# Performance work log

Measured on AMD Instinct MI355X. Metric: run time of the kernel, lower is better.

The kernel has to match this reference:

```python
import jax, jax.numpy as jnp
import numpy as np


def gcn_conv(x, edge_index, edge_weight, W, b):
    """PyG GCNConv: add self-loops (weight 1), symmetric normalization,
    linear transform, edge-weighted scatter-add aggregation, bias."""
    N = x.shape[0]
    src = jnp.concatenate([edge_index[0], jnp.arange(N, dtype=edge_index.dtype)])
    dst = jnp.concatenate([edge_index[1], jnp.arange(N, dtype=edge_index.dtype)])
    ew = jnp.concatenate([edge_weight, jnp.ones((N,), dtype=edge_weight.dtype)])
    # deg over destination nodes (source_to_target flow)
    deg = jax.ops.segment_sum(ew, dst, num_segments=N)
    dinv = jnp.where(deg > 0, deg ** -0.5, 0.0).astype(x.dtype)
    norm = dinv[src] * ew * dinv[dst]          # [E+N]
    xw = x @ W                                  # [N, out] linear first (cheaper)
    msgs = norm[:, None] * xw[src]              # [E+N, out]
    out = jax.ops.segment_sum(msgs, dst, num_segments=N)
    return out + b


def setup_inputs() -> dict:
    key = jax.random.key(0)
    ks = jax.random.split(key, 7)
    N, E, F_in, H, F_out = 100000, 1600000, 394, 256, 64
    x = jax.random.normal(ks[0], (N, F_in), dtype=jnp.float32)
    edge_index = jax.random.randint(ks[1], (2, E), 0, N, dtype=jnp.int32)
    edge_weight = jax.random.uniform(ks[2], (E,), dtype=jnp.float32)
    W1 = jax.random.normal(ks[3], (F_in, H), dtype=jnp.float32) * (1.0 / np.sqrt(F_in))
    b1 = jnp.zeros((H,), dtype=jnp.float32)
    W2 = jax.random.normal(ks[4], (H, F_out), dtype=jnp.float32) * (1.0 / np.sqrt(H))
    b2 = jnp.zeros((F_out,), dtype=jnp.float32)
    return {"x": x, "edge_index": edge_index, "edge_weight": edge_weight,
            "W1": W1, "b1": b1, "W2": W2, "b2": b2}


def reference(x, edge_index, edge_weight, W1, b1, W2, b2):
    h = gcn_conv(x, edge_index, edge_weight, W1, b1)
    h = jax.nn.relu(h)
    # F.dropout(training=self.training) is identity in eval mode
    out = gcn_conv(h, edge_index, edge_weight, W2, b2)
    return out
```

## Files before the change

### kernel.cpp

```cpp
#include <hip/hip_runtime.h>
#include <hip/hip_bf16.h>
#include <hip/hip_fp16.h>
#include <type_traits>


typedef _Float16 f16x8 __attribute__((ext_vector_type(8)));
typedef float f32x4 __attribute__((ext_vector_type(4)));

#define DEG_MASK ((1ull << 42) - 1)

__device__ inline void async_copy16(const void* g, void* l) {
    __builtin_amdgcn_global_load_lds(
        (const __attribute__((address_space(1))) void*)g,
        (__attribute__((address_space(3))) void*)l, 16, 0, 0);
}


__global__ __launch_bounds__(256) void init_node(unsigned long long* packed, int N) {
    int i = blockIdx.x * 256 + threadIdx.x;
    if (i < N) packed[i] = 0ull;
}

__global__ __launch_bounds__(256) void accum_deg_hist(const int* __restrict__ dst,
                                                      const float* __restrict__ ew,
                                                      unsigned long long* packed, int E) {
    int e = blockIdx.x * 256 + threadIdx.x;
    if (e < E) {
        int d = dst[e];
        unsigned long long add =
            (1ull << 42) + (unsigned long long)(ew[e] * 4294967296.0f);
        atomicAdd(&packed[d], add);
    }
}

#define SCAN_TILE 2048

__global__ __launch_bounds__(256) void scan1(const unsigned long long* __restrict__ packed,
                                             int* __restrict__ rowptr,
                                             float* __restrict__ dinv,
                                             int* __restrict__ bsums, int N) {
    __shared__ int tmp[256];
    int t = threadIdx.x;
    int base = blockIdx.x * SCAN_TILE + t * 8;
    int v[8], s = 0;
#pragma unroll
    for (int j = 0; j < 8; ++j) {
        int idx = base + j;
        if (idx < N) {
            unsigned long long pv = packed[idx];
            v[j] = (int)(pv >> 42);
            dinv[idx] = rsqrtf(1.0f + (float)(pv & DEG_MASK) * (1.0f / 4294967296.0f));
        } else v[j] = 0;
        s += v[j];
    }
    tmp[t] = s;
    __syncthreads();
#pragma unroll
    for (int off = 1; off < 256; off <<= 1) {
        int u = (t >= off) ? tmp[t - off] : 0;
        __syncthreads();
        tmp[t] += u;
        __syncthreads();
    }
    int run = tmp[t] - s;
#pragma unroll
    for (int j = 0; j < 8; ++j) {
        if (base + j < N) rowptr[base + j] = run;
        run += v[j];
    }
    if (t == 255) bsums[blockIdx.x] = tmp[255];
}

__global__ __launch_bounds__(256) void scan2(int* bsums, int* rowptr, int NB, int N, int E) {
    __shared__ int tmp[256];
    int t = threadIdx.x;
    int v = (t < NB) ? bsums[t] : 0;
    tmp[t] = v;
    __syncthreads();
#pragma unroll
    for (int off = 1; off < 256; off <<= 1) {
        int u = (t >= off) ? tmp[t - off] : 0;
        __syncthreads();
        tmp[t] += u;
        __syncthreads();
    }
    if (t < NB) bsums[t] = tmp[t] - v;
    if (t == 0) rowptr[N] = E;
}

__global__ __launch_bounds__(256) void scan3(int* rowptr, int* cursor,
                                             const int* __restrict__ bsums, int N) {
    int base = blockIdx.x * SCAN_TILE + threadIdx.x * 8;
    int off = bsums[blockIdx.x];
#pragma unroll
    for (int j = 0; j < 8; ++j)
        if (base + j < N) {
            int v = rowptr[base + j] + off;
            rowptr[base + j] = v;
            cursor[base + j] = v;
        }
}

__global__ __launch_bounds__(256) void fill_csr(const int* __restrict__ src,
                                                const int* __restrict__ dst,
                                                const float* __restrict__ ew,
                                                const float* __restrict__ dinv,
                                                int* __restrict__ cursor,
                                                int2* __restrict__ cv, int E) {
    int e = blockIdx.x * 256 + threadIdx.x;
    if (e < E) {
        int d = dst[e], s = src[e];
        int pos = atomicAdd(&cursor[d], 1);
        float v = dinv[s] * ew[e] * dinv[d];
        cv[pos] = make_int2(s, __float_as_int(v));
    }
}

__global__ __launch_bounds__(256) void tohalf_w(const float* __restrict__ W,
                                                __half* __restrict__ WT,
                                                int K, int N, int Kpad) {
    int idx = blockIdx.x * 256 + threadIdx.x;
    int total = N * Kpad;
    if (idx >= total) return;
    int n = idx / Kpad, k = idx % Kpad;
    float v = (k < K) ? W[(size_t)k * N + n] : 0.0f;
    WT[idx] = __float2half(v);
}

__global__ __launch_bounds__(256) void tohalf_x(const float* __restrict__ x,
                                                __half* __restrict__ Xh,
                                                int Nn, int K, int Kpad) {
    int idx = blockIdx.x * 256 + threadIdx.x;
    int cpr = Kpad / 8;
    int total = Nn * cpr;
    if (idx >= total) return;
    int row = idx / cpr, c = idx % cpr;
    int gk = c * 8;
    const float* p = x + (size_t)row * K + gk;
    float v[8];
    if (gk + 8 <= K) {
#pragma unroll
        for (int j = 0; j < 4; ++j) {
            float2 t2 = *(const float2*)(p + j * 2);
            v[j * 2] = t2.x; v[j * 2 + 1] = t2.y;
        }
    } else {
#pragma unroll
        for (int j = 0; j < 8; ++j) v[j] = (gk + j < K) ? p[j] : 0.0f;
    }
    union { __half2 h[4]; uint4 u; } pk;
#pragma unroll
    for (int j = 0; j < 4; ++j) pk.h[j] = __floats2half2_rn(v[j * 2], v[j * 2 + 1]);
    *(uint4*)&Xh[(size_t)row * Kpad + gk] = pk.u;
}

template <int BM, int BN, int WARPS_M, int WARPS_N, int NT>
__global__ __launch_bounds__(NT) void gemm_f16(const __half* __restrict__ Ah,
                                               const __half* __restrict__ BT,
                                               __half* __restrict__ C,
                                               int M, int Kpad) {
    const int WM = BM / WARPS_M, WN = BN / WARPS_N;
    const int FM = WM / 16, FN = WN / 16;
    const int ACH = BM * 4;
    const int BCH = BN * 4;
    const int TOTCH = ACH + BCH;
    const int CH = TOTCH / NT;
    static_assert(CH == 3, "vmcnt(3) hardcoded below");
    __shared__ __align__(16) __half lds[2][TOTCH * 8];

    int tid = threadIdx.x;
    int lane = tid & 63;
    int w = tid >> 6;
    int wr = w / WARPS_N, wc = w % WARPS_N;
    int bm = blockIdx.x * BM;
    int lrow = lane & 15;
    int lslot = lane >> 4;

    const __half* srcp[CH];
#pragma unroll
    for (int i = 0; i < CH; ++i) {
        int ch = tid + i * NT;
        if (ch < ACH) {
            int c = ch, row = c >> 2;
            int grow = bm + row;
            if (grow >= M) grow = M - 1;
            srcp[i] = Ah + (size_t)grow * Kpad + (size_t)(((c & 3) ^ ((row >> 1) & 3)) * 8);
        } else {
            int c = ch - ACH, row = c >> 2;
            srcp[i] = BT + (size_t)row * Kpad + (size_t)(((c & 3) ^ ((row >> 1) & 3)) * 8);
        }
    }

    f32x4 acc[FM][FN];
#pragma unroll
    for (int m = 0; m < FM; ++m)
#pragma unroll
        for (int n = 0; n < FN; ++n) acc[m][n] = (f32x4){0.f, 0.f, 0.f, 0.f};

    auto stage = [&](int buf) {
#pragma unroll
        for (int i = 0; i < CH; ++i) {
            async_copy16(srcp[i], &lds[buf][(size_t)((tid & ~63) + i * NT) * 8]);
            srcp[i] += 32;
        }
    };

    auto compute = [&](int buf) {
        f16x8 af[FM], bf[FN];
#pragma unroll
        for (int m = 0; m < FM; ++m) {
            int row = wr * WM + m * 16 + lrow;
            int p = lslot ^ ((row >> 1) & 3);
            af[m] = *(const f16x8*)&lds[buf][(size_t)(row * 4 + p) * 8];
        }
#pragma unroll
        for (int n = 0; n < FN; ++n) {
            int row = wc * WN + n * 16 + lrow;
            int p = lslot ^ ((row >> 1) & 3);
            bf[n] = *(const f16x8*)&lds[buf][(size_t)(ACH + row * 4 + p) * 8];
        }
#pragma unroll
        for (int m = 0; m < FM; ++m)
#pragma unroll
            for (int n = 0; n < FN; ++n)
                acc[m][n] = __builtin_amdgcn_mfma_f32_16x16x32_f16(af[m], bf[n], acc[m][n], 0, 0, 0);
    };

    const int nsteps = Kpad / 32;
    stage(0);
    for (int s = 0; s < nsteps; ++s) {
        if (s + 1 < nsteps) {
            stage((s + 1) & 1);
            asm volatile("s_waitcnt vmcnt(3)" ::: "memory");
        } else {
            asm volatile("s_waitcnt vmcnt(0)" ::: "memory");
        }
        __builtin_amdgcn_s_barrier();
        compute(s & 1);
        __builtin_amdgcn_s_barrier();
    }

    __syncthreads();
    {
        const int LW = WN + 8;
        __half* tile = (__half*)lds + (size_t)w * 16 * LW;
        const int CPR = WN / 8;
        const int CHT = (16 * CPR) / 64;
#pragma unroll
        for (int m = 0; m < FM; ++m) {
            int rb = bm + wr * WM + m * 16;
#pragma unroll
            for (int n = 0; n < FN; ++n)
#pragma unroll
                for (int i = 0; i < 4; ++i)
                    tile[((lane >> 4) * 4 + i) * LW + n * 16 + (lane & 15)] =
                        __float2half(acc[m][n][i]);
#pragma unroll
            for (int c = 0; c < CHT; ++c) {
                int ch = lane + c * 64;
                int r = ch / CPR, cc = ch % CPR;
                uint4 v = *(uint4*)&tile[r * LW + cc * 8];
                int grow = rb + r;
                if (grow < M)
                    *(uint4*)&C[(size_t)grow * BN + wc * WN + cc * 8] = v;
            }
        }
    }
}

template <int F, int LPN, int RELU, typename OutT>
__global__ __launch_bounds__(256) void gatherh(const int* __restrict__ rowptr,
                                               const int2* __restrict__ cv,
                                               const __half* __restrict__ xw,
                                               const float* __restrict__ dinv,
                                               const float* __restrict__ bias,
                                               OutT* __restrict__ out, int N) {
    const int NPB = 256 / LPN;
    int d = blockIdx.x * NPB + threadIdx.x / LPN;
    if (d >= N) return;
    int lane = threadIdx.x % LPN;

    float di = dinv[d];
    float w = di * di;
    uint2 raw = *(const uint2*)(xw + (size_t)d * F + lane * 4);
    float2 u0 = __half22float2(*(__half2*)&raw.x);
    float2 u1 = __half22float2(*(__half2*)&raw.y);
    float a0 = w * u0.x, a1 = w * u0.y, a2 = w * u1.x, a3 = w * u1.y;
    float b0 = 0.f, b1 = 0.f, b2 = 0.f, b3 = 0.f;

    int p = rowptr[d], p1 = rowptr[d + 1];
    for (; p + 4 <= p1; p += 4) {
        int2 e0 = cv[p], e1 = cv[p + 1], e2 = cv[p + 2], e3 = cv[p + 3];
        uint2 r0 = *(const uint2*)(xw + (size_t)e0.x * F + lane * 4);
        uint2 r1 = *(const uint2*)(xw + (size_t)e1.x * F + lane * 4);
        uint2 r2 = *(const uint2*)(xw + (size_t)e2.x * F + lane * 4);
        uint2 r3 = *(const uint2*)(xw + (size_t)e3.x * F + lane * 4);
        float w0 = __int_as_float(e0.y), w1 = __int_as_float(e1.y);
        float w2 = __int_as_float(e2.y), w3 = __int_as_float(e3.y);
        {
            float2 v0 = __half22float2(*(__half2*)&r0.x);
            float2 v1 = __half22float2(*(__half2*)&r0.y);
            a0 = fmaf(w0, v0.x, a0); a1 = fmaf(w0, v0.y, a1);
            a2 = fmaf(w0, v1.x, a2); a3 = fmaf(w0, v1.y, a3);
        }
        {
            float2 v0 = __half22float2(*(__half2*)&r1.x);
            float2 v1 = __half22float2(*(__half2*)&r1.y);
            b0 = fmaf(w1, v0.x, b0); b1 = fmaf(w1, v0.y, b1);
            b2 = fmaf(w1, v1.x, b2); b3 = fmaf(w1, v1.y, b3);
        }
        {
            float2 v0 = __half22float2(*(__half2*)&r2.x);
            float2 v1 = __half22float2(*(__half2*)&r2.y);
            a0 = fmaf(w2, v0.x, a0); a1 = fmaf(w2, v0.y, a1);
            a2 = fmaf(w2, v1.x, a2); a3 = fmaf(w2, v1.y, a3);
        }
        {
            float2 v0 = __half22float2(*(__half2*)&r3.x);
            float2 v1 = __half22float2(*(__half2*)&r3.y);
            b0 = fmaf(w3, v0.x, b0); b1 = fmaf(w3, v0.y, b1);
            b2 = fmaf(w3, v1.x, b2); b3 = fmaf(w3, v1.y, b3);
        }
    }
    for (; p < p1; ++p) {
        int2 e = cv[p];
        float wv = __int_as_float(e.y);
        uint2 rv = *(const uint2*)(xw + (size_t)e.x * F + lane * 4);
        float2 v0 = __half22float2(*(__half2*)&rv.x);
        float2 v1 = __half22float2(*(__half2*)&rv.y);
        a0 = fmaf(wv, v0.x, a0); a1 = fmaf(wv, v0.y, a1);
        a2 = fmaf(wv, v1.x, a2); a3 = fmaf(wv, v1.y, a3);
    }
    a0 += b0; a1 += b1; a2 += b2; a3 += b3;

    float4 bb = *(const float4*)&bias[lane * 4];
    a0 += bb.x; a1 += bb.y; a2 += bb.z; a3 += bb.w;
    if (RELU) {
        a0 = fmaxf(a0, 0.f); a1 = fmaxf(a1, 0.f);
        a2 = fmaxf(a2, 0.f); a3 = fmaxf(a3, 0.f);
    }
    if constexpr (std::is_same_v<OutT, float>) {
        *(float4*)&out[(size_t)d * F + lane * 4] = make_float4(a0, a1, a2, a3);
    } else {
        __half2 h0 = __floats2half2_rn(a0, a1);
        __half2 h1 = __floats2half2_rn(a2, a3);
        uint2 packed;
        packed.x = *(uint*)&h0;
        packed.y = *(uint*)&h1;
        *(uint2*)&out[(size_t)d * F + lane * 4] = packed;
    }
}

extern "C" void kernel_launch(void* const* d_in, const int* in_sizes, int n_in,
                              void* d_out, int out_size, void* d_ws, size_t ws_size,
                              hipStream_t stream) {
    const float* x  = (const float*)d_in[0];
    const int*   ei = (const int*)d_in[1];
    const float* ew = (const float*)d_in[2];
    const float* W1 = (const float*)d_in[3];
    const float* b1 = (const float*)d_in[4];
    const float* W2 = (const float*)d_in[5];
    const float* b2 = (const float*)d_in[6];
    float* out = (float*)d_out;

    const int H    = in_sizes[4];
    const int Fout = in_sizes[6];
    const int Fin  = in_sizes[3] / H;
    const int N    = in_sizes[0] / Fin;
    const int E    = in_sizes[2];

    const int Kpad1 = (Fin + 31) / 32 * 32;
    const int Kpad2 = (H + 31) / 32 * 32;

    const int* src = ei;
    const int* dst = ei + E;

    unsigned long long* packed = (unsigned long long*)d_ws;
    float* dinv   = (float*)(packed + N);
    int*   rowptr = (int*)(dinv + N);
    int*   cursor = rowptr + N + 4;
    int*   bsums  = cursor + N + 4;
    int2*  cv     = (int2*)(bsums + 256);
    __half* bufA  = (__half*)(cv + E);
    __half* bufB  = bufA + (size_t)N * H;
    __half* xh    = bufB + (size_t)N * H;
    __half* wt1   = xh + (size_t)N * Kpad1;
    __half* wt2   = wt1 + (size_t)H * Kpad1;

    const int NB = (N + SCAN_TILE - 1) / SCAN_TILE;

    init_node<<<(N + 255) / 256, 256, 0, stream>>>(packed, N);
    accum_deg_hist<<<(E + 255) / 256, 256, 0, stream>>>(dst, ew, packed, E);

    scan1<<<NB, 256, 0, stream>>>(packed, rowptr, dinv, bsums, N);
    scan2<<<1, 256, 0, stream>>>(bsums, rowptr, NB, N, E);
    scan3<<<NB, 256, 0, stream>>>(rowptr, cursor, bsums, N);
    fill_csr<<<(E + 255) / 256, 256, 0, stream>>>(src, dst, ew, dinv, cursor, cv, E);

    tohalf_w<<<(H * Kpad1 + 255) / 256, 256, 0, stream>>>(W1, wt1, Fin, H, Kpad1);
    tohalf_w<<<(Fout * Kpad2 + 255) / 256, 256, 0, stream>>>(W2, wt2, H, Fout, Kpad2);
    tohalf_x<<<((size_t)N * (Kpad1 / 8) + 255) / 256, 256, 0, stream>>>(x, xh, N, Fin, Kpad1);

    gemm_f16<128, 256, 2, 4, 512><<<(N + 127) / 128, 512, 0, stream>>>(xh, wt1, bufA, N, Kpad1);

    gatherh<256, 64, 1, __half><<<(N + 3) / 4, 256, 0, stream>>>(
        rowptr, cv, bufA, dinv, b1, bufB, N);

    gemm_f16<128, 64, 2, 2, 256><<<(N + 127) / 128, 256, 0, stream>>>(bufB, wt2, bufA, N, Kpad2);

    gatherh<64, 16, 0, float><<<(N + 15) / 16, 256, 0, stream>>>(
        rowptr, cv, bufA, dinv, b2, out, N);
}
```

Before: 476.3 us.

## Fuse fp32-to-fp16 conversion of x into first GEMM's A-tile loading

Removes the separate tohalf_x pass and its fp16 staging buffer. The first-layer GEMM now reads fp32 x rows directly into registers, converts them to fp16 and writes them into swizzled LDS, while B tiles still use async global-to-LDS copies. This saves a full write and re-read of the converted x matrix. In exchange, A loads go through registers with explicit waitcnt handling instead of the async LDS path, which could weaken latency hiding in the GEMM main loop.

Measured after the change: 466.8 us. 2.0% less time.

```diff
diff --git a/kernel.cpp b/kernel.cpp
--- a/kernel.cpp
+++ b/kernel.cpp
@@ -127,31 +127,145 @@
     WT[idx] = __float2half(v);
 }
 
-__global__ __launch_bounds__(256) void tohalf_x(const float* __restrict__ x,
-                                                __half* __restrict__ Xh,
-                                                int Nn, int K, int Kpad) {
-    int idx = blockIdx.x * 256 + threadIdx.x;
-    int cpr = Kpad / 8;
-    int total = Nn * cpr;
-    if (idx >= total) return;
-    int row = idx / cpr, c = idx % cpr;
-    int gk = c * 8;
-    const float* p = x + (size_t)row * K + gk;
-    float v[8];
-    if (gk + 8 <= K) {
-#pragma unroll
-        for (int j = 0; j < 4; ++j) {
-            float2 t2 = *(const float2*)(p + j * 2);
-            v[j * 2] = t2.x; v[j * 2 + 1] = t2.y;
-        }
-    } else {
-#pragma unroll
-        for (int j = 0; j < 8; ++j) v[j] = (gk + j < K) ? p[j] : 0.0f;
-    }
-    union { __half2 h[4]; uint4 u; } pk;
-#pragma unroll
-    for (int j = 0; j < 4; ++j) pk.h[j] = __floats2half2_rn(v[j * 2], v[j * 2 + 1]);
-    *(uint4*)&Xh[(size_t)row * Kpad + gk] = pk.u;
+template <int BM, int BN, int WARPS_M, int WARPS_N, int NT>
+__global__ __launch_bounds__(NT) void gemm_f32a(const float* __restrict__ Ax,
+                                                const __half* __restrict__ BT,
+                                                __half* __restrict__ C,
+                                                int M, int K, int Kpad) {
+    const int WM = BM / WARPS_M, WN = BN / WARPS_N;
+    const int FM = WM / 16, FN = WN / 16;
+    const int ACH = BM * 4;
+    const int BCH = BN * 4;
+    static_assert(ACH == NT, "1 A-chunk per thread");
+    static_assert(BCH == 2 * NT, "2 B-chunks per thread");
+    __shared__ __align__(16) __half lds[2][(ACH + BCH) * 8];
+
+    int tid = threadIdx.x;
+    int lane = tid & 63;
+    int w = tid >> 6;
+    int wr = w / WARPS_N, wc = w % WARPS_N;
+    int bm = blockIdx.x * BM;
+    int lrow = lane & 15;
+    int lslot = lane >> 4;
+
+    int arow = tid >> 2, ap = tid & 3;
+    int aslot = ap ^ ((arow >> 1) & 3);
+    int agrow = bm + arow; if (agrow >= M) agrow = M - 1;
+    const float* abase = Ax + (size_t)agrow * K;
+
+    const __half* bsrc[2];
+#pragma unroll
+    for (int i = 0; i < 2; ++i) {
+        int c = tid + i * NT;
+        int row = c >> 2, p = c & 3;
+        bsrc[i] = BT + (size_t)row * Kpad + (size_t)((p ^ ((row >> 1) & 3)) * 8);
+    }
+
+    f32x4 acc[FM][FN];
+#pragma unroll
+    for (int m = 0; m < FM; ++m)
+#pragma unroll
+        for (int n = 0; n < FN; ++n) acc[m][n] = (f32x4){0.f, 0.f, 0.f, 0.f};
+
+    float2 ar[4];
+    auto loadA = [&](int s) {
+        int gk = s * 32 + aslot * 8;
+        if (gk + 8 <= K) {
+            const float* p = abase + gk;
+            ar[0] = *(const float2*)p;
+            ar[1] = *(const float2*)(p + 2);
+            ar[2] = *(const float2*)(p + 4);
+            ar[3] = *(const float2*)(p + 6);
+        } else {
+            float t[8];
+#pragma unroll
+            for (int j = 0; j < 8; ++j) t[j] = (gk + j < K) ? abase[gk + j] : 0.0f;
+            ar[0] = make_float2(t[0], t[1]);
+            ar[1] = make_float2(t[2], t[3]);
+            ar[2] = make_float2(t[4], t[5]);
+            ar[3] = make_float2(t[6], t[7]);
+        }
+    };
+    auto writeA = [&](int buf) {
+        union { __half2 h[4]; uint4 u; } pk;
+#pragma unroll
+        for (int j = 0; j < 4; ++j) pk.h[j] = __floats2half2_rn(ar[j].x, ar[j].y);
+        *(uint4*)&lds[buf][(size_t)tid * 8] = pk.u;
+    };
+    auto stageB = [&](int buf) {
+#pragma unroll
+        for (int i = 0; i < 2; ++i) {
+            async_copy16(bsrc[i], &lds[buf][(size_t)((tid & ~63) + (i + 1) * NT) * 8]);
+            bsrc[i] += 32;
+        }
+    };
+
+    auto compute = [&](int buf) {
+        f16x8 af[FM], bf[FN];
+#pragma unroll
+        for (int m = 0; m < FM; ++m) {
+            int row = wr * WM + m * 16 + lrow;
+            int p = lslot ^ ((row >> 1) & 3);
+            af[m] = *(const f16x8*)&lds[buf][(size_t)(row * 4 + p) * 8];
+        }
+#pragma unroll
+        for (int n = 0; n < FN; ++n) {
+            int row = wc * WN + n * 16 + lrow;
+            int p = lslot ^ ((row >> 1) & 3);
+            bf[n] = *(const f16x8*)&lds[buf][(size_t)(ACH + row * 4 + p) * 8];
+        }
+#pragma unroll
+        for (int m = 0; m < FM; ++m)
+#pragma unroll
+            for (int n = 0; n < FN; ++n)
+                acc[m][n] = __builtin_amdgcn_mfma_f32_16x16x32_f16(af[m], bf[n], acc[m][n], 0, 0, 0);
+    };
+
+    const int nsteps = Kpad / 32;
+    loadA(0);
+    stageB(0);
+    asm volatile("s_waitcnt vmcnt(2)" ::: "memory");
+    writeA(0);
+    asm volatile("s_waitcnt vmcnt(0) lgkmcnt(0)" ::: "memory");
+    __builtin_amdgcn_s_barrier();
+    for (int s = 0; s < nsteps; ++s) {
+        bool more = (s + 1 < nsteps);
+        if (more) { loadA(s + 1); stageB((s + 1) & 1); }
+        compute(s & 1);
+        if (more) {
+            asm volatile("s_waitcnt vmcnt(2)" ::: "memory");
+            writeA((s + 1) & 1);
+            asm volatile("s_waitcnt vmcnt(0) lgkmcnt(0)" ::: "memory");
+        }
+        __builtin_amdgcn_s_barrier();
+    }
+
+    __syncthreads();
+    {
+        const int LW = WN + 8;
+        __half* tile = (__half*)lds + (size_t)w * 16 * LW;
+        const int CPR = WN / 8;
+        const int CHT = (16 * CPR) / 64;
+#pragma unroll
+        for (int m = 0; m < FM; ++m) {
+            int rb = bm + wr * WM + m * 16;
+#pragma unroll
+            for (int n = 0; n < FN; ++n)
+#pragma unroll
+                for (int i = 0; i < 4; ++i)
+                    tile[((lane >> 4) * 4 + i) * LW + n * 16 + (lane & 15)] =
+                        __float2half(acc[m][n][i]);
+#pragma unroll
+            for (int c = 0; c < CHT; ++c) {
+                int ch = lane + c * 64;
+                int r = ch / CPR, cc = ch % CPR;
+                uint4 v = *(uint4*)&tile[r * LW + cc * 8];
+                int grow = rb + r;
+                if (grow < M)
+                    *(uint4*)&C[(size_t)grow * BN + wc * WN + cc * 8] = v;
+            }
+        }
+    }
 }
 
 template <int BM, int BN, int WARPS_M, int WARPS_N, int NT>
@@ -383,8 +497,7 @@
     int2*  cv     = (int2*)(bsums + 256);
     __half* bufA  = (__half*)(cv + E);
     __half* bufB  = bufA + (size_t)N * H;
-    __half* xh    = bufB + (size_t)N * H;
-    __half* wt1   = xh + (size_t)N * Kpad1;
+    __half* wt1   = bufB + (size_t)N * H;
     __half* wt2   = wt1 + (size_t)H * Kpad1;
 
     const int NB = (N + SCAN_TILE - 1) / SCAN_TILE;
@@ -399,9 +512,9 @@
 
     tohalf_w<<<(H * Kpad1 + 255) / 256, 256, 0, stream>>>(W1, wt1, Fin, H, Kpad1);
     tohalf_w<<<(Fout * Kpad2 + 255) / 256, 256, 0, stream>>>(W2, wt2, H, Fout, Kpad2);
-    tohalf_x<<<((size_t)N * (Kpad1 / 8) + 255) / 256, 256, 0, stream>>>(x, xh, N, Fin, Kpad1);
-
-    gemm_f16<128, 256, 2, 4, 512><<<(N + 127) / 128, 512, 0, stream>>>(xh, wt1, bufA, N, Kpad1);
+
+    gemm_f32a<128, 256, 2, 4, 512><<<(N + 127) / 128, 512, 0, stream>>>(
+        x, wt1, bufA, N, Fin, Kpad1);
 
     gatherh<256, 64, 1, __half><<<(N + 3) / 4, 256, 0, stream>>>(
         rowptr, cv, bufA, dinv, b1, bufB, N);
```
